# Kernel tuning notes

Hardware: AMD Instinct MI355X
Metric: run time of the kernel (lower is better)

## Reference

```python
import jax, jax.numpy as jnp
import numpy as np

B, SQ, SK, D, H = 4, 2048, 2048, 1024, 16
HD = D // H


def setup_inputs() -> dict:
    key = jax.random.key(0)
    ks = jax.random.split(key, 12)
    s = 1.0 / np.sqrt(D)
    return {
        "query": jax.random.normal(ks[0], (B, SQ, D), jnp.float32),
        "key": jax.random.normal(ks[1], (B, SK, D), jnp.float32),
        "value": jax.random.normal(ks[2], (B, SK, D), jnp.float32),
        "key_padding_mask": jax.random.randint(ks[3], (B, SK), 0, 2, jnp.int32),
        "Wq": jax.random.uniform(ks[4], (D, D), jnp.float32, -s, s),
        "bq": jnp.zeros((D,), jnp.float32),
        "Wk": jax.random.uniform(ks[5], (D, D), jnp.float32, -s, s),
        "bk": jnp.zeros((D,), jnp.float32),
        "Wv": jax.random.uniform(ks[6], (D, D), jnp.float32, -s, s),
        "bv": jnp.zeros((D,), jnp.float32),
        "Wo": jax.random.uniform(ks[7], (D, D), jnp.float32, -s, s),
        "bo": jnp.zeros((D,), jnp.float32),
    }


def reference(query, key, value, key_padding_mask, Wq, bq, Wk, bk, Wv, bv, Wo, bo):
    scale = HD ** -0.5
    # projections: torch Linear is x @ W.T + b
    q = (query @ Wq.T + bq).reshape(B, SQ, H, HD).transpose(0, 2, 1, 3)  # [B,H,SQ,HD]
    k = (key @ Wk.T + bk).reshape(B, SK, H, HD).transpose(0, 2, 1, 3)    # [B,H,SK,HD]
    v = (value @ Wv.T + bv).reshape(B, SK, H, HD).transpose(0, 2, 1, 3)  # [B,H,SK,HD]
    scores = jnp.einsum("bhqd,bhkd->bhqk", q, k) * scale                  # [B,H,SQ,SK]
    mask = key_padding_mask[:, None, None, :] != 0                        # True = keep
    scores = jnp.where(mask, scores, -jnp.inf)
    attn = jax.nn.softmax(scores, axis=-1)
    # dropout is identity at inference (eval mode)
    out = jnp.einsum("bhqk,bhkd->bhqd", attn, v)                          # [B,H,SQ,HD]
    out = out.transpose(0, 2, 1, 3).reshape(B, SQ, D)
    return out @ Wo.T + bo
```

## Files before the change

kernel.cpp:

```cpp
#include <hip/hip_runtime.h>


typedef __bf16 bf16_t;
typedef __attribute__((ext_vector_type(4))) __bf16 bf16x4;
typedef __attribute__((ext_vector_type(8))) __bf16 bf16x8;
typedef __attribute__((ext_vector_type(4))) float f32x4;

#define MFMA16(a, b, c) __builtin_amdgcn_mfma_f32_16x16x32_bf16(a, b, c, 0, 0, 0)

#define WAITV(N) asm volatile("s_waitcnt vmcnt(" #N ")" ::: "memory")

__device__ __forceinline__ void gl_lds16(const void* g, void* l) {
  __builtin_amdgcn_global_load_lds(
      (const __attribute__((address_space(1))) unsigned int*)g,
      (__attribute__((address_space(3))) unsigned int*)l, 16, 0, 0);
}

__device__ __forceinline__ void block_barrier() {
  asm volatile("" ::: "memory");
  __builtin_amdgcn_s_barrier();
  asm volatile("" ::: "memory");
}

__global__ void wconv_kernel(const float* __restrict__ Wq, const float* __restrict__ Wk,
                             const float* __restrict__ Wv, const float* __restrict__ Wo,
                             bf16_t* __restrict__ out) {
  const int m = blockIdx.y;
  const float* src = (m == 0) ? Wq : (m == 1) ? Wk : (m == 2) ? Wv : Wo;
  bf16_t* dst = out + (size_t)m * (1024 * 1024);
  const int idx = (blockIdx.x * 256 + threadIdx.x) * 4;
  float4 v = *(const float4*)(src + idx);
  bf16x4 pk;
  pk[0] = (bf16_t)v.x; pk[1] = (bf16_t)v.y; pk[2] = (bf16_t)v.z; pk[3] = (bf16_t)v.w;
  *(bf16x4*)(dst + idx) = pk;
}

__global__ void iconv_kernel(const float* __restrict__ src, bf16_t* __restrict__ dst) {
  const size_t idx = ((size_t)blockIdx.x * 256 + threadIdx.x) * 4;
  float4 v = *(const float4*)(src + idx);
  bf16x4 pk;
  pk[0] = (bf16_t)v.x; pk[1] = (bf16_t)v.y; pk[2] = (bf16_t)v.z; pk[3] = (bf16_t)v.w;
  *(bf16x4*)(dst + idx) = pk;
}

__global__ __launch_bounds__(256, 2) void gemm_kernel(
    const bf16_t* __restrict__ A, const bf16_t* __restrict__ Bw,
    const float* __restrict__ bias, void* __restrict__ outp, const int out_mode) {
  __shared__ __align__(16) bf16_t As[4][8 * 512];
  __shared__ __align__(16) bf16_t Bs[4][8 * 512];

  const int tid = threadIdx.x;
  const int lane = tid & 63, wave = tid >> 6;
  const int fm = lane & 15, quad = lane >> 4;
  const int wr = wave >> 1, wc = wave & 1;
  const int m0 = blockIdx.x * 128, n0 = blockIdx.y * 128;

  f32x4 acc[4][4];
#pragma unroll
  for (int i = 0; i < 4; ++i)
#pragma unroll
    for (int j = 0; j < 4; ++j) acc[i][j] = f32x4{0.f, 0.f, 0.f, 0.f};

  auto stage = [&](int ks, int buf) {
    const int k0 = ks * 32;
#pragma unroll
    for (int it = 0; it < 2; ++it) {
      const int fid = wave * 2 + it;
      gl_lds16(A + (size_t)(m0 + fid * 16 + fm) * 1024 + k0 + quad * 8,
               As[buf] + fid * 512);
    }
#pragma unroll
    for (int it = 0; it < 2; ++it) {
      const int fid = wave * 2 + it;
      gl_lds16(Bw + (size_t)(n0 + fid * 16 + fm) * 1024 + k0 + quad * 8,
               Bs[buf] + fid * 512);
    }
  };

  stage(0, 0);
  stage(1, 1);
  stage(2, 2);
  for (int ks = 0; ks < 32; ++ks) {
    if (ks <= 29) {
      WAITV(8);
    } else if (ks == 30) {
      WAITV(4);
    } else {
      WAITV(0);
    }
    block_barrier();
    if (ks + 3 < 32) stage(ks + 3, (ks + 3) & 3);
    const bf16_t* Ab = As[ks & 3];
    const bf16_t* Bb = Bs[ks & 3];
    bf16x8 af[4], bfr[4];
#pragma unroll
    for (int i = 0; i < 4; ++i)
      af[i] = *(const bf16x8*)(Ab + (4 * wr + i) * 512 + lane * 8);
#pragma unroll
    for (int j = 0; j < 4; ++j)
      bfr[j] = *(const bf16x8*)(Bb + (4 * wc + j) * 512 + lane * 8);
#pragma unroll
    for (int i = 0; i < 4; ++i)
#pragma unroll
      for (int j = 0; j < 4; ++j) acc[i][j] = MFMA16(af[i], bfr[j], acc[i][j]);
  }

  float bval[4];
#pragma unroll
  for (int j = 0; j < 4; ++j) bval[j] = bias[n0 + wc * 64 + j * 16 + fm];

#pragma unroll
  for (int i = 0; i < 4; ++i) {
#pragma unroll
    for (int j = 0; j < 4; ++j) {
      const int col = n0 + wc * 64 + j * 16 + fm;
#pragma unroll
      for (int r = 0; r < 4; ++r) {
        const int row = m0 + wr * 64 + i * 16 + quad * 4 + r;
        const float v = acc[i][j][r] + bval[j];
        if (out_mode == 2) {
          ((float*)outp)[(size_t)row * 1024 + col] = v;
        } else if (out_mode == 0) {
          ((bf16_t*)outp)[(size_t)row * 1024 + col] = (bf16_t)v;
        } else {
          const int bb = row >> 11, sk = row & 2047;
          const int tt = sk >> 7, L128 = sk & 127;
          const int c = L128 >> 5, hf = (L128 >> 4) & 1;
          const int qd = (L128 >> 2) & 3, rr = L128 & 3;
          const int hh = col >> 6, hd = col & 63;
          const int nt = hd >> 4, fv = hd & 15;
          const size_t idx = (((size_t)(bb * 16 + hh)) << 17) + tt * 8192 +
                             (nt * 4 + c) * 512 + (qd * 16 + fv) * 8 + hf * 4 + rr;
          ((bf16_t*)outp)[idx] = (bf16_t)v;
        }
      }
    }
  }
}

__global__ __launch_bounds__(256, 2) void attn_kernel(
    const bf16_t* __restrict__ q16, const bf16_t* __restrict__ k16,
    const bf16_t* __restrict__ vt16, const int* __restrict__ mask,
    bf16_t* __restrict__ o16) {
  __shared__ __align__(16) bf16_t Kb[2][8192];
  __shared__ __align__(16) bf16_t Vb[2][8192];
  __shared__ float mbuf[2][128];
  __shared__ float lbuf[128];

  const int tid = threadIdx.x;
  const int lane = tid & 63, wave = tid >> 6;
  const int fm = lane & 15, quad = lane >> 4;
  const int lin = blockIdx.y * 16 + blockIdx.x;
  const int xcd = lin & 7, slot = lin >> 3;
  const int qt = slot & 15;
  const int bh = ((slot >> 4) << 3) + xcd;
  const int b = bh >> 4, h = bh & 15;
  const float SC = 0.125f * 1.44269504f;

  bf16x8 aq[2][2];
#pragma unroll
  for (int i = 0; i < 2; ++i)
#pragma unroll
    for (int dc = 0; dc < 2; ++dc) {
      const int row = qt * 128 + (2 * wave + i) * 16 + fm;
      aq[i][dc] = *(const bf16x8*)(q16 + ((size_t)(b * 2048 + row)) * 1024 + h * 64 +
                                   dc * 32 + quad * 8);
    }

  auto stageKV = [&](int t, int buf) {
    const bf16_t* kb = k16 + ((size_t)(b * 2048 + t * 128)) * 1024 + h * 64;
#pragma unroll
    for (int s = 0; s < 4; ++s) {
      const int fid = wave * 4 + s;
      const int row = (fid >> 1) * 16 + fm;
      const int col = (fid & 1) * 32 + quad * 8;
      gl_lds16(kb + (size_t)row * 1024 + col, Kb[buf] + fid * 512);
    }
    const bf16_t* vbase = vt16 + ((size_t)bh << 17) + t * 8192;
#pragma unroll
    for (int s = 0; s < 4; ++s) {
      const int fid = wave * 4 + s;
      gl_lds16(vbase + fid * 512 + lane * 8, Vb[buf] + fid * 512);
    }
    if (tid < 128) mbuf[buf][tid] = mask[b * 2048 + t * 128 + tid] ? 0.0f : -1e30f;
  };

  f32x4 oacc[2][4];
#pragma unroll
  for (int i = 0; i < 2; ++i)
#pragma unroll
    for (int n = 0; n < 4; ++n) oacc[i][n] = f32x4{0.f, 0.f, 0.f, 0.f};
  float lrow[2] = {0.f, 0.f};

  stageKV(0, 0);
  for (int t = 0; t < 16; ++t) {
    __syncthreads();
    if (t + 1 < 16) stageKV(t + 1, (t + 1) & 1);
    const bf16_t* K = Kb[t & 1];
    const bf16_t* V = Vb[t & 1];
    const float* mb = mbuf[t & 1];

    f32x4 sacc[2][8];
#pragma unroll
    for (int i = 0; i < 2; ++i)
#pragma unroll
      for (int j = 0; j < 8; ++j) sacc[i][j] = f32x4{0.f, 0.f, 0.f, 0.f};
#pragma unroll
    for (int j = 0; j < 8; ++j) {
#pragma unroll
      for (int dc = 0; dc < 2; ++dc) {
        bf16x8 kf = *(const bf16x8*)(K + (j * 2 + dc) * 512 + lane * 8);
        sacc[0][j] = MFMA16(kf, aq[0][dc], sacc[0][j]);
        sacc[1][j] = MFMA16(kf, aq[1][dc], sacc[1][j]);
      }
    }

#pragma unroll
    for (int j = 0; j < 8; ++j) {
      f32x4 md = *(const f32x4*)&mb[j * 16 + quad * 4];
#pragma unroll
      for (int i = 0; i < 2; ++i) {
#pragma unroll
        for (int r = 0; r < 4; ++r) {
          const float p = __builtin_amdgcn_exp2f(fmaf(sacc[i][j][r], SC, md[r]));
          sacc[i][j][r] = p;
          lrow[i] += p;
        }
      }
    }

#pragma unroll
    for (int c = 0; c < 4; ++c) {
      bf16x8 pf[2];
#pragma unroll
      for (int i = 0; i < 2; ++i) {
#pragma unroll
        for (int r = 0; r < 4; ++r) {
          pf[i][r] = (bf16_t)sacc[i][2 * c][r];
          pf[i][4 + r] = (bf16_t)sacc[i][2 * c + 1][r];
        }
      }
#pragma unroll
      for (int n = 0; n < 4; ++n) {
        bf16x8 vv = *(const bf16x8*)(V + (n * 4 + c) * 512 + lane * 8);
        oacc[0][n] = MFMA16(pf[0], vv, oacc[0][n]);
        oacc[1][n] = MFMA16(pf[1], vv, oacc[1][n]);
      }
    }
  }

#pragma unroll
  for (int i = 0; i < 2; ++i) {
    float l = lrow[i];
    l += __shfl_xor(l, 16);
    l += __shfl_xor(l, 32);
    if (quad == 0) lbuf[wave * 32 + i * 16 + fm] = l;
  }
  __syncthreads();
#pragma unroll
  for (int i = 0; i < 2; ++i) {
    f32x4 lv = *(const f32x4*)&lbuf[wave * 32 + i * 16 + quad * 4];
#pragma unroll
    for (int r = 0; r < 4; ++r) {
      const float inv = 1.0f / lv[r];
      const int row = qt * 128 + wave * 32 + i * 16 + quad * 4 + r;
#pragma unroll
      for (int n = 0; n < 4; ++n) {
        o16[((size_t)(b * 2048 + row)) * 1024 + h * 64 + n * 16 + fm] =
            (bf16_t)(oacc[i][n][r] * inv);
      }
    }
  }
}

extern "C" void kernel_launch(void* const* d_in, const int* in_sizes, int n_in,
                              void* d_out, int out_size, void* d_ws, size_t ws_size,
                              hipStream_t stream) {
  const float* query = (const float*)d_in[0];
  const float* key   = (const float*)d_in[1];
  const float* value = (const float*)d_in[2];
  const int* mask    = (const int*)d_in[3];
  const float* Wq = (const float*)d_in[4];
  const float* bq = (const float*)d_in[5];
  const float* Wk = (const float*)d_in[6];
  const float* bk = (const float*)d_in[7];
  const float* Wv = (const float*)d_in[8];
  const float* bv = (const float*)d_in[9];
  const float* Wo = (const float*)d_in[10];
  const float* bo = (const float*)d_in[11];

  const size_t MB = 1024 * 1024;
  char* ws = (char*)d_ws;
  bf16_t* W16     = (bf16_t*)ws;
  bf16_t* q16     = (bf16_t*)(ws + 8 * MB);
  bf16_t* k16     = (bf16_t*)(ws + 24 * MB);
  bf16_t* vt16    = (bf16_t*)(ws + 40 * MB);
  bf16_t* scratch = (bf16_t*)(ws + 56 * MB);

  wconv_kernel<<<dim3(1024, 4), 256, 0, stream>>>(Wq, Wk, Wv, Wo, W16);

  iconv_kernel<<<8192, 256, 0, stream>>>(query, scratch);
  gemm_kernel<<<dim3(64, 8), 256, 0, stream>>>(scratch, W16,           bq, q16,  0);

  iconv_kernel<<<8192, 256, 0, stream>>>(key, scratch);
  gemm_kernel<<<dim3(64, 8), 256, 0, stream>>>(scratch, W16 + 1048576, bk, k16,  0);

  iconv_kernel<<<8192, 256, 0, stream>>>(value, scratch);
  gemm_kernel<<<dim3(64, 8), 256, 0, stream>>>(scratch, W16 + 2097152, bv, vt16, 1);

  attn_kernel<<<dim3(16, 64), 256, 0, stream>>>(q16, k16, vt16, mask, scratch);

  gemm_kernel<<<dim3(64, 8), 256, 0, stream>>>(scratch, W16 + 3145728, bo, d_out, 2);
}
```

Before: 415.5 us.

## Merge all fp32-to-bf16 conversions into one launch and shrink GEMM tiles to 64x128

Replaces four separate conversion launches (weights plus three activations) with one 2D-grid conversion kernel. The projection GEMM tile shrinks from 128x128 to 64x128, using a 1x4 wave layout, per-wave load assignment, fewer accumulators and launch bounds of 3. The GEMM grid doubles to 1024 blocks. The aim is to cut launch overhead and improve occupancy and load balance across CUs. The costs are less data reuse per tile and workspace buffers that are now reused across stages through aliasing.

```diff
diff --git a/kernel.cpp b/kernel.cpp
--- a/kernel.cpp
+++ b/kernel.cpp
@@ -22,58 +22,62 @@
   asm volatile("" ::: "memory");
 }
 
-__global__ void wconv_kernel(const float* __restrict__ Wq, const float* __restrict__ Wk,
-                             const float* __restrict__ Wv, const float* __restrict__ Wo,
-                             bf16_t* __restrict__ out) {
-  const int m = blockIdx.y;
-  const float* src = (m == 0) ? Wq : (m == 1) ? Wk : (m == 2) ? Wv : Wo;
-  bf16_t* dst = out + (size_t)m * (1024 * 1024);
-  const int idx = (blockIdx.x * 256 + threadIdx.x) * 4;
-  float4 v = *(const float4*)(src + idx);
+__global__ void conv_kernel(const float* __restrict__ q, const float* __restrict__ k,
+                            const float* __restrict__ v, const float* __restrict__ Wq,
+                            const float* __restrict__ Wk, const float* __restrict__ Wv,
+                            const float* __restrict__ Wo, bf16_t* __restrict__ q16,
+                            bf16_t* __restrict__ k16, bf16_t* __restrict__ v16,
+                            bf16_t* __restrict__ W16) {
+  const int y = blockIdx.y;
+  const float* src;
+  bf16_t* dst;
+  size_t idx;
+  if (y < 3) {
+    src = (y == 0) ? q : (y == 1) ? k : v;
+    dst = (y == 0) ? q16 : (y == 1) ? k16 : v16;
+    idx = ((size_t)blockIdx.x * 256 + threadIdx.x) * 4;
+  } else {
+    if (blockIdx.x >= 4096) return;
+    const int m = blockIdx.x >> 10;
+    src = (m == 0) ? Wq : (m == 1) ? Wk : (m == 2) ? Wv : Wo;
+    dst = W16 + ((size_t)m << 20);
+    idx = (((size_t)(blockIdx.x & 1023)) * 256 + threadIdx.x) * 4;
+  }
+  float4 w = *(const float4*)(src + idx);
   bf16x4 pk;
-  pk[0] = (bf16_t)v.x; pk[1] = (bf16_t)v.y; pk[2] = (bf16_t)v.z; pk[3] = (bf16_t)v.w;
+  pk[0] = (bf16_t)w.x; pk[1] = (bf16_t)w.y; pk[2] = (bf16_t)w.z; pk[3] = (bf16_t)w.w;
   *(bf16x4*)(dst + idx) = pk;
 }
 
-__global__ void iconv_kernel(const float* __restrict__ src, bf16_t* __restrict__ dst) {
-  const size_t idx = ((size_t)blockIdx.x * 256 + threadIdx.x) * 4;
-  float4 v = *(const float4*)(src + idx);
-  bf16x4 pk;
-  pk[0] = (bf16_t)v.x; pk[1] = (bf16_t)v.y; pk[2] = (bf16_t)v.z; pk[3] = (bf16_t)v.w;
-  *(bf16x4*)(dst + idx) = pk;
-}
-
-__global__ __launch_bounds__(256, 2) void gemm_kernel(
+__global__ __launch_bounds__(256, 3) void gemm_kernel(
     const bf16_t* __restrict__ A, const bf16_t* __restrict__ Bw,
     const float* __restrict__ bias, void* __restrict__ outp, const int out_mode) {
-  __shared__ __align__(16) bf16_t As[4][8 * 512];
+  __shared__ __align__(16) bf16_t As[4][4 * 512];
   __shared__ __align__(16) bf16_t Bs[4][8 * 512];
 
   const int tid = threadIdx.x;
   const int lane = tid & 63, wave = tid >> 6;
   const int fm = lane & 15, quad = lane >> 4;
-  const int wr = wave >> 1, wc = wave & 1;
-  const int m0 = blockIdx.x * 128, n0 = blockIdx.y * 128;
-
-  f32x4 acc[4][4];
+  const int m0 = blockIdx.x * 64, n0 = blockIdx.y * 128;
+
+  f32x4 acc[4][2];
 #pragma unroll
   for (int i = 0; i < 4; ++i)
 #pragma unroll
-    for (int j = 0; j < 4; ++j) acc[i][j] = f32x4{0.f, 0.f, 0.f, 0.f};
+    for (int j = 0; j < 2; ++j) acc[i][j] = f32x4{0.f, 0.f, 0.f, 0.f};
 
   auto stage = [&](int ks, int buf) {
     const int k0 = ks * 32;
 #pragma unroll
-    for (int it = 0; it < 2; ++it) {
-      const int fid = wave * 2 + it;
-      gl_lds16(A + (size_t)(m0 + fid * 16 + fm) * 1024 + k0 + quad * 8,
-               As[buf] + fid * 512);
-    }
-#pragma unroll
-    for (int it = 0; it < 2; ++it) {
-      const int fid = wave * 2 + it;
-      gl_lds16(Bw + (size_t)(n0 + fid * 16 + fm) * 1024 + k0 + quad * 8,
-               Bs[buf] + fid * 512);
+    for (int it = 0; it < 3; ++it) {
+      const int f = wave * 3 + it;
+      if (f < 4) {
+        gl_lds16(A + (size_t)(m0 + f * 16 + fm) * 1024 + k0 + quad * 8,
+                 As[buf] + f * 512);
+      } else {
+        gl_lds16(Bw + (size_t)(n0 + (f - 4) * 16 + fm) * 1024 + k0 + quad * 8,
+                 Bs[buf] + (f - 4) * 512);
+      }
     }
   };
 
@@ -81,10 +85,11 @@
   stage(1, 1);
   stage(2, 2);
   for (int ks = 0; ks < 32; ++ks) {
+    __builtin_amdgcn_sched_barrier(0);
     if (ks <= 29) {
-      WAITV(8);
+      WAITV(6);
     } else if (ks == 30) {
-      WAITV(4);
+      WAITV(3);
     } else {
       WAITV(0);
     }
@@ -92,31 +97,31 @@
     if (ks + 3 < 32) stage(ks + 3, (ks + 3) & 3);
     const bf16_t* Ab = As[ks & 3];
     const bf16_t* Bb = Bs[ks & 3];
-    bf16x8 af[4], bfr[4];
+    bf16x8 af[4], bfr[2];
 #pragma unroll
     for (int i = 0; i < 4; ++i)
-      af[i] = *(const bf16x8*)(Ab + (4 * wr + i) * 512 + lane * 8);
-#pragma unroll
-    for (int j = 0; j < 4; ++j)
-      bfr[j] = *(const bf16x8*)(Bb + (4 * wc + j) * 512 + lane * 8);
+      af[i] = *(const bf16x8*)(Ab + i * 512 + lane * 8);
+#pragma unroll
+    for (int j = 0; j < 2; ++j)
+      bfr[j] = *(const bf16x8*)(Bb + (wave * 2 + j) * 512 + lane * 8);
 #pragma unroll
     for (int i = 0; i < 4; ++i)
 #pragma unroll
-      for (int j = 0; j < 4; ++j) acc[i][j] = MFMA16(af[i], bfr[j], acc[i][j]);
-  }
-
-  float bval[4];
-#pragma unroll
-  for (int j = 0; j < 4; ++j) bval[j] = bias[n0 + wc * 64 + j * 16 + fm];
+      for (int j = 0; j < 2; ++j) acc[i][j] = MFMA16(af[i], bfr[j], acc[i][j]);
+  }
+
+  float bval[2];
+#pragma unroll
+  for (int j = 0; j < 2; ++j) bval[j] = bias[n0 + wave * 32 + j * 16 + fm];
 
 #pragma unroll
   for (int i = 0; i < 4; ++i) {
 #pragma unroll
-    for (int j = 0; j < 4; ++j) {
-      const int col = n0 + wc * 64 + j * 16 + fm;
+    for (int j = 0; j < 2; ++j) {
+      const int col = n0 + wave * 32 + j * 16 + fm;
 #pragma unroll
       for (int r = 0; r < 4; ++r) {
-        const int row = m0 + wr * 64 + i * 16 + quad * 4 + r;
+        const int row = m0 + i * 16 + quad * 4 + r;
         const float v = acc[i][j][r] + bval[j];
         if (out_mode == 2) {
           ((float*)outp)[(size_t)row * 1024 + col] = v;
@@ -291,24 +296,25 @@
 
   const size_t MB = 1024 * 1024;
   char* ws = (char*)d_ws;
-  bf16_t* W16     = (bf16_t*)ws;
-  bf16_t* q16     = (bf16_t*)(ws + 8 * MB);
-  bf16_t* k16     = (bf16_t*)(ws + 24 * MB);
-  bf16_t* vt16    = (bf16_t*)(ws + 40 * MB);
-  bf16_t* scratch = (bf16_t*)(ws + 56 * MB);
-
-  wconv_kernel<<<dim3(1024, 4), 256, 0, stream>>>(Wq, Wk, Wv, Wo, W16);
-
-  iconv_kernel<<<8192, 256, 0, stream>>>(query, scratch);
-  gemm_kernel<<<dim3(64, 8), 256, 0, stream>>>(scratch, W16,           bq, q16,  0);
-
-  iconv_kernel<<<8192, 256, 0, stream>>>(key, scratch);
-  gemm_kernel<<<dim3(64, 8), 256, 0, stream>>>(scratch, W16 + 1048576, bk, k16,  0);
-
-  iconv_kernel<<<8192, 256, 0, stream>>>(value, scratch);
-  gemm_kernel<<<dim3(64, 8), 256, 0, stream>>>(scratch, W16 + 2097152, bv, vt16, 1);
-
-  attn_kernel<<<dim3(16, 64), 256, 0, stream>>>(q16, k16, vt16, mask, scratch);
-
-  gemm_kernel<<<dim3(64, 8), 256, 0, stream>>>(scratch, W16 + 3145728, bo, d_out, 2);
-}
+  bf16_t* W16 = (bf16_t*)ws;
+  bf16_t* qin = (bf16_t*)(ws + 8 * MB);
+  bf16_t* kin = (bf16_t*)(ws + 24 * MB);
+  bf16_t* vin = (bf16_t*)(ws + 40 * MB);
+  bf16_t* q16 = (bf16_t*)(ws + 56 * MB);
+
+  conv_kernel<<<dim3(8192, 4), 256, 0, stream>>>(query, key, value, Wq, Wk, Wv, Wo,
+                                                 qin, kin, vin, W16);
+
+  gemm_kernel<<<dim3(128, 8), 256, 0, stream>>>(qin, W16, bq, q16, 0);
+
+  bf16_t* k16 = qin;
+  gemm_kernel<<<dim3(128, 8), 256, 0, stream>>>(kin, W16 + 1048576, bk, k16, 0);
+
+  bf16_t* vt16 = kin;
+  gemm_kernel<<<dim3(128, 8), 256, 0, stream>>>(vin, W16 + 2097152, bv, vt16, 1);
+
+  bf16_t* o16 = vin;
+  attn_kernel<<<dim3(16, 64), 256, 0, stream>>>(q16, k16, vt16, mask, o16);
+
+  gemm_kernel<<<dim3(128, 8), 256, 0, stream>>>(o16, W16 + 3145728, bo, d_out, 2);
+}
```

Measured after the change: 442.1 us. 1.06x slower.

## Batch input conversions and QKV projections into single launches

Applied to the files above, without the earlier changes.

All fp32→bf16 conversions (query, key, value and the four weights) now run in one conversion kernel, and the three Q/K/V projection GEMMs run as one launch using blockIdx.z to select operands. This removes several kernel launches and the serialization between them, and gives the projection GEMM three times as many blocks to fill the GPU. To fit the extra buffers it reuses the output buffer as scratch for K and V^T, which assumes the final GEMM does not overwrite them while they are still being read. The conversion grid launches idle blocks for the weight row beyond 4096.

```diff
diff --git a/kernel.cpp b/kernel.cpp
--- a/kernel.cpp
+++ b/kernel.cpp
@@ -22,32 +22,48 @@
   asm volatile("" ::: "memory");
 }
 
-__global__ void wconv_kernel(const float* __restrict__ Wq, const float* __restrict__ Wk,
-                             const float* __restrict__ Wv, const float* __restrict__ Wo,
-                             bf16_t* __restrict__ out) {
-  const int m = blockIdx.y;
-  const float* src = (m == 0) ? Wq : (m == 1) ? Wk : (m == 2) ? Wv : Wo;
-  bf16_t* dst = out + (size_t)m * (1024 * 1024);
-  const int idx = (blockIdx.x * 256 + threadIdx.x) * 4;
-  float4 v = *(const float4*)(src + idx);
+__global__ void conv_kernel(const float* __restrict__ q, const float* __restrict__ k,
+                            const float* __restrict__ v, const float* __restrict__ Wq,
+                            const float* __restrict__ Wk, const float* __restrict__ Wv,
+                            const float* __restrict__ Wo, bf16_t* __restrict__ q16,
+                            bf16_t* __restrict__ k16, bf16_t* __restrict__ v16,
+                            bf16_t* __restrict__ W16) {
+  const int y = blockIdx.y;
+  const float* src;
+  bf16_t* dst;
+  size_t idx;
+  if (y < 3) {
+    src = (y == 0) ? q : (y == 1) ? k : v;
+    dst = (y == 0) ? q16 : (y == 1) ? k16 : v16;
+    idx = ((size_t)blockIdx.x * 256 + threadIdx.x) * 4;
+  } else {
+    if (blockIdx.x >= 4096) return;
+    const int m = blockIdx.x >> 10;
+    src = (m == 0) ? Wq : (m == 1) ? Wk : (m == 2) ? Wv : Wo;
+    dst = W16 + ((size_t)m << 20);
+    idx = (((size_t)(blockIdx.x & 1023)) * 256 + threadIdx.x) * 4;
+  }
+  float4 w = *(const float4*)(src + idx);
   bf16x4 pk;
-  pk[0] = (bf16_t)v.x; pk[1] = (bf16_t)v.y; pk[2] = (bf16_t)v.z; pk[3] = (bf16_t)v.w;
+  pk[0] = (bf16_t)w.x; pk[1] = (bf16_t)w.y; pk[2] = (bf16_t)w.z; pk[3] = (bf16_t)w.w;
   *(bf16x4*)(dst + idx) = pk;
 }
 
-__global__ void iconv_kernel(const float* __restrict__ src, bf16_t* __restrict__ dst) {
-  const size_t idx = ((size_t)blockIdx.x * 256 + threadIdx.x) * 4;
-  float4 v = *(const float4*)(src + idx);
-  bf16x4 pk;
-  pk[0] = (bf16_t)v.x; pk[1] = (bf16_t)v.y; pk[2] = (bf16_t)v.z; pk[3] = (bf16_t)v.w;
-  *(bf16x4*)(dst + idx) = pk;
-}
-
 __global__ __launch_bounds__(256, 2) void gemm_kernel(
-    const bf16_t* __restrict__ A, const bf16_t* __restrict__ Bw,
-    const float* __restrict__ bias, void* __restrict__ outp, const int out_mode) {
+    const bf16_t* __restrict__ A0, const bf16_t* __restrict__ A1,
+    const bf16_t* __restrict__ A2, const bf16_t* __restrict__ Wbase,
+    const float* __restrict__ b0, const float* __restrict__ b1,
+    const float* __restrict__ b2, void* __restrict__ o0, void* __restrict__ o1,
+    void* __restrict__ o2, const int md0, const int md1, const int md2) {
   __shared__ __align__(16) bf16_t As[4][8 * 512];
   __shared__ __align__(16) bf16_t Bs[4][8 * 512];
+
+  const int z = blockIdx.z;
+  const bf16_t* A = (z == 0) ? A0 : (z == 1) ? A1 : A2;
+  const bf16_t* Bw = Wbase + ((size_t)z << 20);
+  const float* bias = (z == 0) ? b0 : (z == 1) ? b1 : b2;
+  void* outp = (z == 0) ? o0 : (z == 1) ? o1 : o2;
+  const int out_mode = (z == 0) ? md0 : (z == 1) ? md1 : md2;
 
   const int tid = threadIdx.x;
   const int lane = tid & 63, wave = tid >> 6;
@@ -291,24 +307,25 @@
 
   const size_t MB = 1024 * 1024;
   char* ws = (char*)d_ws;
-  bf16_t* W16     = (bf16_t*)ws;
-  bf16_t* q16     = (bf16_t*)(ws + 8 * MB);
-  bf16_t* k16     = (bf16_t*)(ws + 24 * MB);
-  bf16_t* vt16    = (bf16_t*)(ws + 40 * MB);
-  bf16_t* scratch = (bf16_t*)(ws + 56 * MB);
-
-  wconv_kernel<<<dim3(1024, 4), 256, 0, stream>>>(Wq, Wk, Wv, Wo, W16);
-
-  iconv_kernel<<<8192, 256, 0, stream>>>(query, scratch);
-  gemm_kernel<<<dim3(64, 8), 256, 0, stream>>>(scratch, W16,           bq, q16,  0);
-
-  iconv_kernel<<<8192, 256, 0, stream>>>(key, scratch);
-  gemm_kernel<<<dim3(64, 8), 256, 0, stream>>>(scratch, W16 + 1048576, bk, k16,  0);
-
-  iconv_kernel<<<8192, 256, 0, stream>>>(value, scratch);
-  gemm_kernel<<<dim3(64, 8), 256, 0, stream>>>(scratch, W16 + 2097152, bv, vt16, 1);
-
-  attn_kernel<<<dim3(16, 64), 256, 0, stream>>>(q16, k16, vt16, mask, scratch);
-
-  gemm_kernel<<<dim3(64, 8), 256, 0, stream>>>(scratch, W16 + 3145728, bo, d_out, 2);
-}
+  bf16_t* W16 = (bf16_t*)ws;
+  bf16_t* qin = (bf16_t*)(ws + 8 * MB);
+  bf16_t* kin = (bf16_t*)(ws + 24 * MB);
+  bf16_t* vin = (bf16_t*)(ws + 40 * MB);
+  bf16_t* q16 = (bf16_t*)(ws + 56 * MB);
+
+  bf16_t* k16  = (bf16_t*)d_out;
+  bf16_t* vt16 = (bf16_t*)((char*)d_out + 16 * MB);
+  bf16_t* o16  = qin;
+
+  conv_kernel<<<dim3(8192, 4), 256, 0, stream>>>(query, key, value, Wq, Wk, Wv, Wo,
+                                                 qin, kin, vin, W16);
+
+  gemm_kernel<<<dim3(64, 8, 3), 256, 0, stream>>>(
+      qin, kin, vin, W16, bq, bk, bv, q16, k16, vt16, 0, 0, 1);
+
+  attn_kernel<<<dim3(16, 64), 256, 0, stream>>>(q16, k16, vt16, mask, o16);
+
+  gemm_kernel<<<dim3(64, 8, 1), 256, 0, stream>>>(
+      o16, nullptr, nullptr, W16 + 3145728, bo, nullptr, nullptr, d_out, nullptr,
+      nullptr, 2, 0, 0);
+}
```

Result: faster. 394.8 us (-5.0%).
